# Performance work log

Hardware: AMD Instinct MI355X
Metric: run time of the kernel (lower is better)

Reference implementation:

```python
import jax, jax.numpy as jnp
import numpy as np

B, N, G = 16, 6000, 256
T = 200                     # TRAIN_ROIS_PER_IMAGE
RATIO = 0.33                # POSITIVE_ROI_RATIO
POS_NUM = int(T * RATIO)    # 66 positive slots
NEG_SLOTS = T - POS_NUM     # 134 negative slots
BBOX_STD = jnp.asarray([0.1, 0.1, 0.2, 0.2], jnp.float32)
EPS = 1e-8


def _rand_boxes(key, b, n):
    # valid [y1,x1,y2,x2] boxes in [0,1]
    k1, k2 = jax.random.split(key)
    tl = jax.random.uniform(k1, (b, n, 2)) * 0.7
    wh = jax.random.uniform(k2, (b, n, 2)) * 0.25 + 0.02
    return jnp.concatenate([tl, tl + wh], axis=-1).astype(jnp.float32)


def setup_inputs() -> dict:
    key = jax.random.key(0)
    k1, k2, k3, k4, k5 = jax.random.split(key, 5)
    rois = _rand_boxes(k1, B, N)
    rois = rois.at[:, N - 1000:].set(0.0)          # zero padding tail (remove_zero_padding)
    gt_boxes = _rand_boxes(k2, B, G)
    gt_ids = jax.random.randint(k3, (B, G), 1, 81, dtype=jnp.int32)
    gt_ids = gt_ids.at[:, G - 32:G - 16].set(-1)   # crowd boxes (ids < 0)
    gt_ids = gt_ids.at[:, G - 16:].set(0)          # padded gt
    gt_boxes = gt_boxes.at[:, G - 16:].set(0.0)
    pos_score = jax.random.uniform(k4, (B, N), dtype=jnp.float32)
    neg_score = jax.random.uniform(k5, (B, N), dtype=jnp.float32)
    return {"rois": rois, "gt_ids": gt_ids, "gt_boxes": gt_boxes,
            "pos_score": pos_score, "neg_score": neg_score}


def _pairwise_iou(a, b):
    # a:[N,4], b:[G,4] -> [N,G]
    y1 = jnp.maximum(a[:, None, 0], b[None, :, 0])
    x1 = jnp.maximum(a[:, None, 1], b[None, :, 1])
    y2 = jnp.minimum(a[:, None, 2], b[None, :, 2])
    x2 = jnp.minimum(a[:, None, 3], b[None, :, 3])
    inter = jnp.clip(y2 - y1, 0.0) * jnp.clip(x2 - x1, 0.0)
    area_a = (a[:, 2] - a[:, 0]) * (a[:, 3] - a[:, 1])
    area_b = (b[:, 2] - b[:, 0]) * (b[:, 3] - b[:, 1])
    union = area_a[:, None] + area_b[None, :] - inter
    return inter / jnp.maximum(union, EPS)


def _bbox_offset(boxes, gt):
    h = jnp.maximum(boxes[:, 2] - boxes[:, 0], EPS)
    w = jnp.maximum(boxes[:, 3] - boxes[:, 1], EPS)
    cy = boxes[:, 0] + 0.5 * h
    cx = boxes[:, 1] + 0.5 * w
    gh = jnp.maximum(gt[:, 2] - gt[:, 0], EPS)
    gw = jnp.maximum(gt[:, 3] - gt[:, 1], EPS)
    gcy = gt[:, 0] + 0.5 * gh
    gcx = gt[:, 1] + 0.5 * gw
    off = jnp.stack([(gcy - cy) / h, (gcx - cx) / w,
                     jnp.log(gh / h), jnp.log(gw / w)], axis=1)
    return off / BBOX_STD


def _per_image(rois, gt_ids, gt_boxes, pos_score, neg_score):
    roi_valid = jnp.any(rois != 0.0, axis=1)        # [N]
    gt_valid = jnp.any(gt_boxes != 0.0, axis=1)     # [G]
    crowd = gt_valid & (gt_ids < 0)
    non_crowd = gt_valid & (gt_ids > 0)

    iou = _pairwise_iou(rois, gt_boxes)             # [N,G]
    iou_nc = jnp.where(non_crowd[None, :], iou, -1.0)
    iou_nc_max = jnp.max(iou_nc, axis=1)
    iou_cr_max = jnp.max(jnp.where(crowd[None, :], iou, 0.0), axis=1)

    pos_mask = roi_valid & (iou_nc_max >= 0.5)
    neg_mask = roi_valid & (iou_nc_max < 0.5) & (iou_cr_max < 0.001)

    # random sampling == sort by iid uniform scores (masked out -> -inf)
    pos_idx = jnp.argsort(-jnp.where(pos_mask, pos_score, -jnp.inf))[:POS_NUM]
    pos_count = jnp.minimum(jnp.sum(pos_mask), POS_NUM).astype(jnp.int32)
    pos_slot_valid = jnp.arange(POS_NUM) < pos_count

    neg_target = (jnp.float32(1.0 / RATIO) * pos_count.astype(jnp.float32)).astype(jnp.int32) - pos_count
    neg_idx = jnp.argsort(-jnp.where(neg_mask, neg_score, -jnp.inf))[:NEG_SLOTS]
    neg_count = jnp.minimum(jnp.sum(neg_mask).astype(jnp.int32),
                            jnp.minimum(neg_target, NEG_SLOTS))
    neg_slot_valid = jnp.arange(NEG_SLOTS) < neg_count

    pos_rois_raw = rois[pos_idx]                                   # [P,4]
    pos_rois = jnp.where(pos_slot_valid[:, None], pos_rois_raw, 0.0)
    neg_rois = jnp.where(neg_slot_valid[:, None], rois[neg_idx], 0.0)

    assign = jnp.argmax(iou_nc[pos_idx], axis=1)                   # gt assignment
    roi_gt_boxes = gt_boxes[assign]
    roi_gt_ids = jnp.where(pos_slot_valid, gt_ids[assign], 0)

    off = _bbox_offset(pos_rois_raw, roi_gt_boxes)
    off = jnp.where(pos_slot_valid[:, None], off, 0.0)

    out_rois = jnp.concatenate([pos_rois, neg_rois], axis=0)       # [T,4]
    out_ids = jnp.pad(roi_gt_ids, (0, NEG_SLOTS))                  # [T]
    out_off = jnp.pad(off, ((0, NEG_SLOTS), (0, 0)))               # [T,4]
    return out_rois, out_ids, out_off


def reference(rois, gt_ids, gt_boxes, pos_score, neg_score):
    return jax.vmap(_per_image)(rois, gt_ids, gt_boxes, pos_score, neg_score)
```

## Files before the change

### kernel.cpp

```cpp
#include <hip/hip_runtime.h>

#define BIMG 16
#define NROI 6000
#define NGT  256
#define TPOS 66
#define TNEG 134
#define TTOT 200
#define EPSF 1e-8f
#define INVALID_SCORE 0xFFFFFFFFu

typedef unsigned long long u64;
typedef unsigned int u32;
typedef unsigned char u8;

__global__ __launch_bounds__(256)
void iou_keys_kernel(const float* __restrict__ rois,
                     const int* __restrict__ gt_ids,
                     const float* __restrict__ gt_boxes,
                     const float* __restrict__ pos_score,
                     const float* __restrict__ neg_score,
                     u32* __restrict__ pos_s,
                     u32* __restrict__ neg_s,
                     u8* __restrict__ assign)
{
#pragma clang fp contract(off)
    const int b = blockIdx.y;
    __shared__ float4 s_box[NGT];
    __shared__ float2 s_af[NGT];
    {
        const int g = threadIdx.x;
        float4 gb = ((const float4*)gt_boxes)[b * NGT + g];
        s_box[g] = gb;
        float area = (gb.z - gb.x) * (gb.w - gb.y);
        bool valid = (gb.x != 0.f) || (gb.y != 0.f) || (gb.z != 0.f) || (gb.w != 0.f);
        int id = gt_ids[b * NGT + g];
        float flag = valid ? (id > 0 ? 1.f : (id < 0 ? 2.f : 0.f)) : 0.f;
        s_af[g] = make_float2(area, flag);
    }
    __syncthreads();

    const int r_local = threadIdx.x >> 3;
    const int sub = threadIdx.x & 7;
    const int n = blockIdx.x * 32 + r_local;
    const int n_eff = min(n, NROI - 1);

    float4 rb = ((const float4*)rois)[b * NROI + n_eff];
    const bool rvalid = (rb.x != 0.f) || (rb.y != 0.f) || (rb.z != 0.f) || (rb.w != 0.f);
    const float area_a = (rb.z - rb.x) * (rb.w - rb.y);

    float best = -1.0f;
    int bestg = sub;
    float crmax = 0.0f;

    for (int gg = 0; gg < 32; ++gg) {
        const int g = (gg << 3) | sub;
        float4 p0 = s_box[g];
        float2 af = s_af[g];
        float y1 = fmaxf(rb.x, p0.x);
        float x1 = fmaxf(rb.y, p0.y);
        float y2 = fminf(rb.z, p0.z);
        float x2 = fminf(rb.w, p0.w);
        float ih = fmaxf(y2 - y1, 0.0f);
        float iw = fmaxf(x2 - x1, 0.0f);
        float inter = ih * iw;
        float uni = fmaxf(area_a + af.x - inter, EPSF);
        float iou = inter / uni;
        float vnc = (af.y == 1.f) ? iou : -1.0f;
        if (vnc > best) { best = vnc; bestg = g; }
        float vcr = (af.y == 2.f) ? iou : 0.0f;
        crmax = fmaxf(crmax, vcr);
    }

    for (int m = 1; m <= 4; m <<= 1) {
        float ov = __shfl_xor(best, m);
        int   og = __shfl_xor(bestg, m);
        float oc = __shfl_xor(crmax, m);
        if (ov > best || (ov == best && og < bestg)) { best = ov; bestg = og; }
        crmax = fmaxf(crmax, oc);
    }

    if (sub == 0 && n < NROI) {
        u32 ps = INVALID_SCORE, ns = INVALID_SCORE;
        if (rvalid) {
            if (best >= 0.5f)
                ps = __float_as_uint(pos_score[b * NROI + n]);
            if ((best < 0.5f) && (crmax < 0.001f))
                ns = __float_as_uint(neg_score[b * NROI + n]);
        }
        pos_s[b * NROI + n] = ps;
        neg_s[b * NROI + n] = ns;
        assign[b * NROI + n] = (u8)bestg;
    }
}

#define BSEL 512
#define SLOTS 12

__device__ __forceinline__ int radix_select(const u32* __restrict__ src, int K,
                                            int tid, int lane, int w,
                                            u32* s_hist, u32* s_wtot, u32* s_wsuf,
                                            int* s_pick, u32* s_higher,
                                            int* s_count, u64* s_comp, int* s_cnt,
                                            int* s_sel )
{
    u32 sc[SLOTS];
    int myvalid = 0;
    for (int s = 0; s < SLOTS; ++s) {
        int idx = s * BSEL + tid;
        sc[s] = (idx < NROI) ? src[idx] : INVALID_SCORE;
        myvalid += (sc[s] != INVALID_SCORE);
    }
    for (int off = 1; off < 64; off <<= 1) myvalid += __shfl_xor(myvalid, off);
    if (tid == 0) *s_count = 0;
    __syncthreads();
    if (lane == 0) atomicAdd(s_count, (u32)myvalid);
    __syncthreads();
    const int total = *s_count;
    int Krem = min(K, total);
    if (Krem <= 0) return total;

    u64 prefix = 0ull, mask = 0ull;
    for (int p = 3; p >= 0; --p) {
        const int shift = p * 11;
        for (int i = tid; i < 2048; i += BSEL) s_hist[i] = 0;
        __syncthreads();
        for (int s = 0; s < SLOTS; ++s) {
            if (sc[s] != INVALID_SCORE) {
                u64 k = ((u64)sc[s] << 13) | (u64)(8191 - (s * BSEL + tid));
                if ((k & mask) == prefix)
                    atomicAdd(&s_hist[(u32)(k >> shift) & 2047u], 1u);
            }
        }
        __syncthreads();
        u32 local = s_hist[4 * tid] + s_hist[4 * tid + 1]
                  + s_hist[4 * tid + 2] + s_hist[4 * tid + 3];
        u32 suf = local;
        for (int off = 1; off < 64; off <<= 1) {
            u32 v = __shfl_down(suf, off);
            if (lane + off < 64) suf += v;
        }
        if (lane == 0) s_wtot[w] = suf;
        __syncthreads();
        if (tid < 8) {
            u32 t = 0;
            for (int j = tid + 1; j < 8; ++j) t += s_wtot[j];
            s_wsuf[tid] = t;
        }
        __syncthreads();
        u32 Sincl = suf + s_wsuf[w];
        for (int k2 = 0; k2 < 4; ++k2) {
            u32 h = s_hist[4 * tid + k2];
            u32 Snext = Sincl - h;
            if (Sincl >= (u32)Krem && Snext < (u32)Krem) {
                *s_pick = 4 * tid + k2;
                *s_higher = Snext;
            }
            Sincl = Snext;
        }
        __syncthreads();
        prefix |= ((u64)(u32)(*s_pick)) << shift;
        mask   |= (2047ull << shift);
        Krem   -= (int)(*s_higher);
        __syncthreads();
    }
    if (tid == 0) *s_cnt = 0;
    __syncthreads();
    for (int s = 0; s < SLOTS; ++s) {
        if (sc[s] != INVALID_SCORE) {
            u64 k = ((u64)sc[s] << 13) | (u64)(8191 - (s * BSEL + tid));
            if (k >= prefix) {
                int pos = atomicAdd(s_cnt, 1);
                s_comp[pos] = k;
            }
        }
    }
    __syncthreads();
    const int Ksel = *s_cnt;
    if (tid < Ksel) {
        u64 k = s_comp[tid];
        int rank = 0;
        for (int j = 0; j < Ksel; ++j) rank += (s_comp[j] > k);
        s_sel[rank] = 8191 - (int)(k & 8191ull);
    }
    __syncthreads();
    return total;
}

__global__ __launch_bounds__(BSEL)
void select_gather_kernel(const float* __restrict__ rois,
                          const int* __restrict__ gt_ids,
                          const float* __restrict__ gt_boxes,
                          const u32* __restrict__ pos_s,
                          const u32* __restrict__ neg_s,
                          const u8* __restrict__ assign,
                          float* __restrict__ out)
{
#pragma clang fp contract(off)
    __shared__ u32 s_hist[2048];
    __shared__ u32 s_wtot[8];
    __shared__ u32 s_wsuf[8];
    __shared__ int s_pick;
    __shared__ u32 s_higher;
    __shared__ int s_count;
    __shared__ u64 s_comp[TNEG];
    __shared__ int s_cnt;
    __shared__ int s_selpos[TPOS];
    __shared__ int s_selneg[TNEG];

    const int b = blockIdx.x;
    const int tid = threadIdx.x;
    const int lane = tid & 63;
    const int w = tid >> 6;

    const int pos_total = radix_select(pos_s + (size_t)b * NROI, TPOS, tid, lane, w,
                                       s_hist, s_wtot, s_wsuf, &s_pick, &s_higher,
                                       &s_count, s_comp, &s_cnt, s_selpos);
    const int pos_count = min(pos_total, TPOS);
    const float ratio_inv = (float)(1.0 / 0.33);
    const int neg_target = (int)(ratio_inv * (float)pos_count) - pos_count;
    const int Kneg = min(neg_target, TNEG);
    int neg_count = 0;
    if (Kneg > 0) {
        const int neg_total = radix_select(neg_s + (size_t)b * NROI, Kneg, tid, lane, w,
                                           s_hist, s_wtot, s_wsuf, &s_pick, &s_higher,
                                           &s_count, s_comp, &s_cnt, s_selneg);
        neg_count = min(neg_total, Kneg);
    }

    if (tid < TTOT) {
        float* out_rois = out;
        float* out_ids  = out + BIMG * TTOT * 4;
        float* out_off  = out + BIMG * TTOT * 4 + BIMG * TTOT;
        const int base = b * TTOT + tid;

        float4 ro  = make_float4(0.f, 0.f, 0.f, 0.f);
        float  idv = 0.f;
        float4 off = make_float4(0.f, 0.f, 0.f, 0.f);

        if (tid < TPOS) {
            if (tid < pos_count) {
                int n = s_selpos[tid];
                float4 rb = ((const float4*)rois)[b * NROI + n];
                ro = rb;
                int g = (int)assign[b * NROI + n];
                float4 gb = ((const float4*)gt_boxes)[b * NGT + g];
                idv = (float)gt_ids[b * NGT + g];

                float h  = fmaxf(rb.z - rb.x, EPSF);
                float wd = fmaxf(rb.w - rb.y, EPSF);
                float cy = rb.x + 0.5f * h;
                float cx = rb.y + 0.5f * wd;
                float gh = fmaxf(gb.z - gb.x, EPSF);
                float gw = fmaxf(gb.w - gb.y, EPSF);
                float gcy = gb.x + 0.5f * gh;
                float gcx = gb.y + 0.5f * gw;
                off.x = ((gcy - cy) / h)  / 0.1f;
                off.y = ((gcx - cx) / wd) / 0.1f;
                off.z = logf(gh / h)  / 0.2f;
                off.w = logf(gw / wd) / 0.2f;
            }
        } else {
            int q = tid - TPOS;
            if (q < neg_count) {
                int n = s_selneg[q];
                ro = ((const float4*)rois)[b * NROI + n];
            }
        }

        ((float4*)out_rois)[base] = ro;
        out_ids[base] = idv;
        ((float4*)out_off)[base] = off;
    }
}

extern "C" void kernel_launch(void* const* d_in, const int* in_sizes, int n_in,
                              void* d_out, int out_size, void* d_ws, size_t ws_size,
                              hipStream_t stream) {
    const float* rois      = (const float*)d_in[0];
    const int*   gt_ids    = (const int*)d_in[1];
    const float* gt_boxes  = (const float*)d_in[2];
    const float* pos_score = (const float*)d_in[3];
    const float* neg_score = (const float*)d_in[4];
    float* out = (float*)d_out;

    char* ws = (char*)d_ws;
    u32* pos_s = (u32*)(ws + 0);
    u32* neg_s = (u32*)(ws + 384000);
    u8*  assign = (u8*)(ws + 768000);

    dim3 gridA((NROI + 31) / 32, BIMG);
    iou_keys_kernel<<<gridA, 256, 0, stream>>>(rois, gt_ids, gt_boxes,
                                               pos_score, neg_score,
                                               pos_s, neg_s, assign);
    select_gather_kernel<<<BIMG, BSEL, 0, stream>>>(rois, gt_ids, gt_boxes,
                                                    pos_s, neg_s, assign, out);
}
```

Baseline: 105.8 us.

## Compact valid GT boxes, split pos/neg selection across blocks, early-exit radix select

Result: faster. 93.38 us (-11.8%).

```diff
diff --git a/kernel.cpp b/kernel.cpp
--- a/kernel.cpp
+++ b/kernel.cpp
@@ -25,19 +25,33 @@
 {
 #pragma clang fp contract(off)
     const int b = blockIdx.y;
-    __shared__ float4 s_box[NGT];
-    __shared__ float2 s_af[NGT];
+    __shared__ float4 s_ncbox[NGT];
+    __shared__ float2 s_ncai[NGT];
+    __shared__ float4 s_crbox[NGT];
+    __shared__ float  s_crarea[NGT];
+    __shared__ int s_nccnt, s_crcnt;
+
+    if (threadIdx.x == 0) { s_nccnt = 0; s_crcnt = 0; }
+    __syncthreads();
     {
         const int g = threadIdx.x;
         float4 gb = ((const float4*)gt_boxes)[b * NGT + g];
-        s_box[g] = gb;
-        float area = (gb.z - gb.x) * (gb.w - gb.y);
         bool valid = (gb.x != 0.f) || (gb.y != 0.f) || (gb.z != 0.f) || (gb.w != 0.f);
         int id = gt_ids[b * NGT + g];
-        float flag = valid ? (id > 0 ? 1.f : (id < 0 ? 2.f : 0.f)) : 0.f;
-        s_af[g] = make_float2(area, flag);
-    }
-    __syncthreads();
+        float area = (gb.z - gb.x) * (gb.w - gb.y);
+        if (valid && id > 0) {
+            int slot = atomicAdd(&s_nccnt, 1);
+            s_ncbox[slot] = gb;
+            s_ncai[slot] = make_float2(area, (float)g);
+        } else if (valid && id < 0) {
+            int slot = atomicAdd(&s_crcnt, 1);
+            s_crbox[slot] = gb;
+            s_crarea[slot] = area;
+        }
+    }
+    __syncthreads();
+    const int nccnt = s_nccnt;
+    const int crcnt = s_crcnt;
 
     const int r_local = threadIdx.x >> 3;
     const int sub = threadIdx.x & 7;
@@ -49,13 +63,12 @@
     const float area_a = (rb.z - rb.x) * (rb.w - rb.y);
 
     float best = -1.0f;
-    int bestg = sub;
+    float bestg = 0.0f;
     float crmax = 0.0f;
 
-    for (int gg = 0; gg < 32; ++gg) {
-        const int g = (gg << 3) | sub;
-        float4 p0 = s_box[g];
-        float2 af = s_af[g];
+    for (int i = sub; i < nccnt; i += 8) {
+        float4 p0 = s_ncbox[i];
+        float2 ai = s_ncai[i];
         float y1 = fmaxf(rb.x, p0.x);
         float x1 = fmaxf(rb.y, p0.y);
         float y2 = fminf(rb.z, p0.z);
@@ -63,19 +76,29 @@
         float ih = fmaxf(y2 - y1, 0.0f);
         float iw = fmaxf(x2 - x1, 0.0f);
         float inter = ih * iw;
-        float uni = fmaxf(area_a + af.x - inter, EPSF);
+        float uni = fmaxf(area_a + ai.x - inter, EPSF);
         float iou = inter / uni;
-        float vnc = (af.y == 1.f) ? iou : -1.0f;
-        if (vnc > best) { best = vnc; bestg = g; }
-        float vcr = (af.y == 2.f) ? iou : 0.0f;
-        crmax = fmaxf(crmax, vcr);
+        bool better = (iou > best) || ((iou == best) && (ai.y < bestg));
+        if (better) { best = iou; bestg = ai.y; }
+    }
+    for (int i = sub; i < crcnt; i += 8) {
+        float4 p0 = s_crbox[i];
+        float y1 = fmaxf(rb.x, p0.x);
+        float x1 = fmaxf(rb.y, p0.y);
+        float y2 = fminf(rb.z, p0.z);
+        float x2 = fminf(rb.w, p0.w);
+        float ih = fmaxf(y2 - y1, 0.0f);
+        float iw = fmaxf(x2 - x1, 0.0f);
+        float inter = ih * iw;
+        float uni = fmaxf(area_a + s_crarea[i] - inter, EPSF);
+        crmax = fmaxf(crmax, inter / uni);
     }
 
     for (int m = 1; m <= 4; m <<= 1) {
         float ov = __shfl_xor(best, m);
-        int   og = __shfl_xor(bestg, m);
+        float og = __shfl_xor(bestg, m);
         float oc = __shfl_xor(crmax, m);
-        if (ov > best || (ov == best && og < bestg)) { best = ov; bestg = og; }
+        if ((ov > best) || ((ov == best) && (og < bestg))) { best = ov; bestg = og; }
         crmax = fmaxf(crmax, oc);
     }
 
@@ -89,19 +112,45 @@
         }
         pos_s[b * NROI + n] = ps;
         neg_s[b * NROI + n] = ns;
-        assign[b * NROI + n] = (u8)bestg;
+        assign[b * NROI + n] = (u8)(int)bestg;
     }
 }
 
 #define BSEL 512
 #define SLOTS 12
+#define CAND_CAP 256
+
+struct SelShared {
+    u32 hist[2048];
+    u32 wtot[8];
+    u32 wsuf[8];
+    int pick;
+    u32 higher;
+    u32 pickpop;
+    u32 count;
+    u64 comp[CAND_CAP];
+    int cnt;
+    int sel[TNEG];
+};
+
+__device__ __forceinline__ int count_valid(const u32* __restrict__ src,
+                                           int tid, int lane, SelShared* S)
+{
+    int myvalid = 0;
+    for (int s = 0; s < SLOTS; ++s) {
+        int idx = s * BSEL + tid;
+        myvalid += (idx < NROI && src[idx] != INVALID_SCORE);
+    }
+    for (int off = 1; off < 64; off <<= 1) myvalid += __shfl_xor(myvalid, off);
+    if (tid == 0) S->count = 0;
+    __syncthreads();
+    if (lane == 0) atomicAdd(&S->count, (u32)myvalid);
+    __syncthreads();
+    return (int)S->count;
+}
 
 __device__ __forceinline__ int radix_select(const u32* __restrict__ src, int K,
-                                            int tid, int lane, int w,
-                                            u32* s_hist, u32* s_wtot, u32* s_wsuf,
-                                            int* s_pick, u32* s_higher,
-                                            int* s_count, u64* s_comp, int* s_cnt,
-                                            int* s_sel )
+                                            int tid, int lane, int w, SelShared* S)
 {
     u32 sc[SLOTS];
     int myvalid = 0;
@@ -111,76 +160,83 @@
         myvalid += (sc[s] != INVALID_SCORE);
     }
     for (int off = 1; off < 64; off <<= 1) myvalid += __shfl_xor(myvalid, off);
-    if (tid == 0) *s_count = 0;
-    __syncthreads();
-    if (lane == 0) atomicAdd(s_count, (u32)myvalid);
-    __syncthreads();
-    const int total = *s_count;
-    int Krem = min(K, total);
-    if (Krem <= 0) return total;
-
+    if (tid == 0) S->count = 0;
+    __syncthreads();
+    if (lane == 0) atomicAdd(&S->count, (u32)myvalid);
+    __syncthreads();
+    const int total = (int)S->count;
+    const int K0 = min(K, total);
+    if (K0 <= 0) return total;
+
+    int Krem = K0;
     u64 prefix = 0ull, mask = 0ull;
+    int cand = total;
+
     for (int p = 3; p >= 0; --p) {
+        if (cand <= CAND_CAP) break;
         const int shift = p * 11;
-        for (int i = tid; i < 2048; i += BSEL) s_hist[i] = 0;
+        for (int i = tid; i < 2048; i += BSEL) S->hist[i] = 0;
         __syncthreads();
         for (int s = 0; s < SLOTS; ++s) {
             if (sc[s] != INVALID_SCORE) {
                 u64 k = ((u64)sc[s] << 13) | (u64)(8191 - (s * BSEL + tid));
                 if ((k & mask) == prefix)
-                    atomicAdd(&s_hist[(u32)(k >> shift) & 2047u], 1u);
-            }
-        }
-        __syncthreads();
-        u32 local = s_hist[4 * tid] + s_hist[4 * tid + 1]
-                  + s_hist[4 * tid + 2] + s_hist[4 * tid + 3];
+                    atomicAdd(&S->hist[(u32)(k >> shift) & 2047u], 1u);
+            }
+        }
+        __syncthreads();
+        u32 local = S->hist[4 * tid] + S->hist[4 * tid + 1]
+                  + S->hist[4 * tid + 2] + S->hist[4 * tid + 3];
         u32 suf = local;
         for (int off = 1; off < 64; off <<= 1) {
             u32 v = __shfl_down(suf, off);
             if (lane + off < 64) suf += v;
         }
-        if (lane == 0) s_wtot[w] = suf;
+        if (lane == 0) S->wtot[w] = suf;
         __syncthreads();
         if (tid < 8) {
             u32 t = 0;
-            for (int j = tid + 1; j < 8; ++j) t += s_wtot[j];
-            s_wsuf[tid] = t;
-        }
-        __syncthreads();
-        u32 Sincl = suf + s_wsuf[w];
+            for (int j = tid + 1; j < 8; ++j) t += S->wtot[j];
+            S->wsuf[tid] = t;
+        }
+        __syncthreads();
+        u32 Sincl = suf + S->wsuf[w];
         for (int k2 = 0; k2 < 4; ++k2) {
-            u32 h = s_hist[4 * tid + k2];
+            u32 h = S->hist[4 * tid + k2];
             u32 Snext = Sincl - h;
             if (Sincl >= (u32)Krem && Snext < (u32)Krem) {
-                *s_pick = 4 * tid + k2;
-                *s_higher = Snext;
+                S->pick = 4 * tid + k2;
+                S->higher = Snext;
+                S->pickpop = h;
             }
             Sincl = Snext;
         }
         __syncthreads();
-        prefix |= ((u64)(u32)(*s_pick)) << shift;
+        prefix |= ((u64)(u32)S->pick) << shift;
         mask   |= (2047ull << shift);
-        Krem   -= (int)(*s_higher);
-        __syncthreads();
-    }
-    if (tid == 0) *s_cnt = 0;
+        Krem   -= (int)S->higher;
+        cand    = (K0 - Krem) + (int)S->pickpop;
+        __syncthreads();
+    }
+
+    if (tid == 0) S->cnt = 0;
     __syncthreads();
     for (int s = 0; s < SLOTS; ++s) {
         if (sc[s] != INVALID_SCORE) {
             u64 k = ((u64)sc[s] << 13) | (u64)(8191 - (s * BSEL + tid));
-            if (k >= prefix) {
-                int pos = atomicAdd(s_cnt, 1);
-                s_comp[pos] = k;
-            }
-        }
-    }
-    __syncthreads();
-    const int Ksel = *s_cnt;
-    if (tid < Ksel) {
-        u64 k = s_comp[tid];
+            if ((k & mask) >= prefix) {
+                int pos = atomicAdd(&S->cnt, 1);
+                S->comp[pos] = k;
+            }
+        }
+    }
+    __syncthreads();
+    const int Cnt = S->cnt;
+    if (tid < Cnt) {
+        u64 k = S->comp[tid];
         int rank = 0;
-        for (int j = 0; j < Ksel; ++j) rank += (s_comp[j] > k);
-        s_sel[rank] = 8191 - (int)(k & 8191ull);
+        for (int j = 0; j < Cnt; ++j) rank += (S->comp[j] > k);
+        if (rank < K0) S->sel[rank] = 8191 - (int)(k & 8191ull);
     }
     __syncthreads();
     return total;
@@ -196,50 +252,29 @@
                           float* __restrict__ out)
 {
 #pragma clang fp contract(off)
-    __shared__ u32 s_hist[2048];
-    __shared__ u32 s_wtot[8];
-    __shared__ u32 s_wsuf[8];
-    __shared__ int s_pick;
-    __shared__ u32 s_higher;
-    __shared__ int s_count;
-    __shared__ u64 s_comp[TNEG];
-    __shared__ int s_cnt;
-    __shared__ int s_selpos[TPOS];
-    __shared__ int s_selneg[TNEG];
-
-    const int b = blockIdx.x;
+    __shared__ SelShared S;
+    const int b = blockIdx.x >> 1;
+    const int side = blockIdx.x & 1;
     const int tid = threadIdx.x;
     const int lane = tid & 63;
     const int w = tid >> 6;
 
-    const int pos_total = radix_select(pos_s + (size_t)b * NROI, TPOS, tid, lane, w,
-                                       s_hist, s_wtot, s_wsuf, &s_pick, &s_higher,
-                                       &s_count, s_comp, &s_cnt, s_selpos);
-    const int pos_count = min(pos_total, TPOS);
-    const float ratio_inv = (float)(1.0 / 0.33);
-    const int neg_target = (int)(ratio_inv * (float)pos_count) - pos_count;
-    const int Kneg = min(neg_target, TNEG);
-    int neg_count = 0;
-    if (Kneg > 0) {
-        const int neg_total = radix_select(neg_s + (size_t)b * NROI, Kneg, tid, lane, w,
-                                           s_hist, s_wtot, s_wsuf, &s_pick, &s_higher,
-                                           &s_count, s_comp, &s_cnt, s_selneg);
-        neg_count = min(neg_total, Kneg);
-    }
-
-    if (tid < TTOT) {
-        float* out_rois = out;
-        float* out_ids  = out + BIMG * TTOT * 4;
-        float* out_off  = out + BIMG * TTOT * 4 + BIMG * TTOT;
-        const int base = b * TTOT + tid;
-
-        float4 ro  = make_float4(0.f, 0.f, 0.f, 0.f);
-        float  idv = 0.f;
-        float4 off = make_float4(0.f, 0.f, 0.f, 0.f);
+    float* out_rois = out;
+    float* out_ids  = out + BIMG * TTOT * 4;
+    float* out_off  = out + BIMG * TTOT * 4 + BIMG * TTOT;
+
+    if (side == 0) {
+        const int pos_total = radix_select(pos_s + (size_t)b * NROI, TPOS,
+                                           tid, lane, w, &S);
+        const int pos_count = min(pos_total, TPOS);
 
         if (tid < TPOS) {
+            const int base = b * TTOT + tid;
+            float4 ro  = make_float4(0.f, 0.f, 0.f, 0.f);
+            float  idv = 0.f;
+            float4 off = make_float4(0.f, 0.f, 0.f, 0.f);
             if (tid < pos_count) {
-                int n = s_selpos[tid];
+                int n = S.sel[tid];
                 float4 rb = ((const float4*)rois)[b * NROI + n];
                 ro = rb;
                 int g = (int)assign[b * NROI + n];
@@ -259,17 +294,31 @@
                 off.z = logf(gh / h)  / 0.2f;
                 off.w = logf(gw / wd) / 0.2f;
             }
-        } else {
-            int q = tid - TPOS;
-            if (q < neg_count) {
-                int n = s_selneg[q];
+            ((float4*)out_rois)[base] = ro;
+            out_ids[base] = idv;
+            ((float4*)out_off)[base] = off;
+        }
+    } else {
+        const int pos_total = count_valid(pos_s + (size_t)b * NROI, tid, lane, &S);
+        const int pos_count = min(pos_total, TPOS);
+        const float ratio_inv = (float)(1.0 / 0.33);
+        const int neg_target = (int)(ratio_inv * (float)pos_count) - pos_count;
+
+        const int neg_total = radix_select(neg_s + (size_t)b * NROI, TNEG,
+                                           tid, lane, w, &S);
+        const int neg_count = max(0, min(neg_total, min(neg_target, TNEG)));
+
+        if (tid < TNEG) {
+            const int base = b * TTOT + TPOS + tid;
+            float4 ro = make_float4(0.f, 0.f, 0.f, 0.f);
+            if (tid < neg_count) {
+                int n = S.sel[tid];
                 ro = ((const float4*)rois)[b * NROI + n];
             }
-        }
-
-        ((float4*)out_rois)[base] = ro;
-        out_ids[base] = idv;
-        ((float4*)out_off)[base] = off;
+            ((float4*)out_rois)[base] = ro;
+            out_ids[base] = 0.f;
+            ((float4*)out_off)[base] = make_float4(0.f, 0.f, 0.f, 0.f);
+        }
     }
 }
 
@@ -292,6 +341,6 @@
     iou_keys_kernel<<<gridA, 256, 0, stream>>>(rois, gt_ids, gt_boxes,
                                                pos_score, neg_score,
                                                pos_s, neg_s, assign);
-    select_gather_kernel<<<BIMG, BSEL, 0, stream>>>(rois, gt_ids, gt_boxes,
-                                                    pos_s, neg_s, assign, out);
-}
+    select_gather_kernel<<<BIMG * 2, BSEL, 0, stream>>>(rois, gt_ids, gt_boxes,
+                                                        pos_s, neg_s, assign, out);
+}
```
